# Kernel optimization log

Hardware: AMD Instinct MI355X
Metric: run time of the kernel (lower is better)

Reference implementation:

```python
import jax, jax.numpy as jnp
import numpy as np
from jax import lax

WINDOW = 512
HOP = 128
SR = 16000
ALPHA = 1e-06
F = WINDOW // 2 + 1  # 257 bins
GAIN = float(np.sqrt(8.0 / 3.0))

# frequency-domain constants (match PsychoacousticMasker properties)
_freqs = np.linspace(0.0, SR / 2.0, F)
_bark_np = 13.0 * np.arctan(0.00076 * _freqs) + 3.5 * np.arctan((_freqs / 7500.0) ** 2)
_valid_dom = (_freqs >= 20.0) & (_freqs <= 20000.0)
_ath_np = np.full(F, -np.inf)
_fk = _freqs[_valid_dom] * 0.001
_ath_np[_valid_dom] = 3.64 * _fk ** -0.8 - 6.5 * np.exp(-0.6 * (_fk - 3.3) ** 2) + 0.001 * _fk ** 4 - 12.0
BARK = jnp.asarray(_bark_np, jnp.float32)
ATH = jnp.asarray(_ath_np, jnp.float32)
DELTA_SHIFT = -6.025 - 0.275 * BARK
HANN = jnp.asarray(0.5 * (1.0 - np.cos(2.0 * np.pi * np.arange(WINDOW) / WINDOW)), jnp.float32)


def _stft(x):
    # center=False hann STFT -> [n_frames, F] complex
    n_frames = (x.shape[0] - WINDOW) // HOP + 1
    idx = jnp.arange(n_frames)[:, None] * HOP + jnp.arange(WINDOW)[None, :]
    return jnp.fft.rfft(x[idx] * HANN, axis=-1)


def _frame_threshold(p):
    # p: [F] SPL-normalized PSD (dB) for one frame -> global masking threshold [F]
    interior = (p[1:-1] > p[:-2]) & (p[1:-1] > p[2:])
    is_max = jnp.pad(interior, (1, 1), constant_values=False)
    pw = 10.0 ** (p / 10.0)
    m_all = 10.0 * jnp.log10(pw + jnp.roll(pw, 1) + jnp.roll(pw, -1))  # tonal masker level (bins j-1,j,j+1)
    valid = is_max & (m_all > ATH)
    order = jnp.argsort((~valid).astype(jnp.int32))  # stable: valid bins first, in frequency order
    vmask = valid[order]
    m_c = jnp.where(vmask, m_all[order], -200.0)     # compacted masker dB values
    n = valid.sum()

    def step(carry, i):
        i_prev, keep = carry
        active = i < n
        # NB: source indexes bark[] with masker *list positions* (i, i_prev); replicated faithfully
        close = (BARK[i] - BARK[i_prev]) < 0.5
        prev_smaller = m_c[i_prev] < m_c[i]
        del_idx = jnp.where(prev_smaller, i_prev, i)
        keep = jnp.where(active & close, keep.at[del_idx].set(False), keep)
        i_prev = jnp.where(active, jnp.where(close, jnp.where(prev_smaller, i_prev + 1, i_prev), i), i_prev)
        return (i_prev, keep), None

    (_, keep), _ = lax.scan(step, (jnp.int32(0), jnp.ones(F, dtype=bool)), jnp.arange(1, F, dtype=jnp.int32))
    keep = keep & vmask
    # individual thresholds, vectorized over maskers k and bins
    z_j = BARK[order]                                    # bark of each masker's bin
    dz = BARK[None, :] - z_j[:, None]                    # [K, F]
    slope = jnp.where(dz > 0, -27.0 + 0.37 * jnp.maximum(m_c - 40.0, 0.0)[:, None], 27.0)
    t = m_c[:, None] + DELTA_SHIFT[order][:, None] + slope * dz
    power = jnp.where(keep[:, None], 10.0 ** (t / 10.0), 0.0)
    return 10.0 * jnp.log10(power.sum(0) + 10.0 ** (ATH / 10.0))


def _threshold_and_psd_max(audio):
    s = _stft(audio)                                     # [T, F]
    psd = 20.0 * jnp.log10(jnp.abs(GAIN * s / WINDOW))
    psd = jnp.maximum(psd, -200.0)
    psd_max = psd.max()
    psd_n = 96.0 - psd_max + psd
    thr = jax.vmap(_frame_threshold)(psd_n)              # [T, F]
    return thr, psd_max


def setup_inputs() -> dict:
    key = jax.random.key(0)
    k1, k2 = jax.random.split(key)
    L = 160000  # 10 s @ 16 kHz; (L - 512) % 128 == 0 -> 1247 frames, pad is a no-op
    x_ref = 0.5 * jax.random.normal(k1, (L,), dtype=jnp.float32)
    x_adv = x_ref + 0.01 * jax.random.normal(k2, (L,), dtype=jnp.float32)
    return {"x_adv": x_adv, "x_ref": x_ref}


def reference(x_adv, x_ref):
    thr, psd_max = _threshold_and_psd_max(x_ref)
    thr = lax.stop_gradient(thr)
    psd_max = lax.stop_gradient(psd_max)
    delta = x_adv - x_ref
    sd = _stft(delta)                                    # [T, F]
    psd_d = (GAIN / WINDOW) ** 2 * (sd.real ** 2 + sd.imag ** 2)
    psd_d = (10.0 ** 9.6) / (10.0 ** (psd_max / 10.0)) * psd_d
    loss = jnp.mean(jax.nn.relu(psd_d - 10.0 ** (thr / 10.0)))
    return ALPHA * loss
```

## Files before the change

### kernel.cpp

```cpp
#include <hip/hip_runtime.h>
#include <math.h>


#define FBINS 257

#define TAB_BARK  0
#define TAB_ATHDB 257
#define TAB_ATHP  514
#define TAB_HANN  771
#define TAB_TWR   1283
#define TAB_TWI   1539
#define TAB_FLOATS 2048

__global__ __launch_bounds__(256) void k0_init(float* __restrict__ tab)
{
    const int tid = threadIdx.x;
    const double TWO_PI = 6.283185307179586476925286766559;
    for (int f = tid; f < FBINS; f += 256) {
        double freq = 31.25 * (double)f;
        double q    = freq / 7500.0;
        tab[TAB_BARK + f] = (float)(13.0 * atan(0.00076 * freq) + 3.5 * atan(q * q));
        if (f == 0) {
            tab[TAB_ATHDB] = -INFINITY;
            tab[TAB_ATHP]  = 0.0f;
        } else {
            double fk = freq * 0.001;
            double ad = 3.64 * pow(fk, -0.8)
                      - 6.5 * exp(-0.6 * (fk - 3.3) * (fk - 3.3))
                      + 0.001 * fk * fk * fk * fk - 12.0;
            float av = (float)ad;
            tab[TAB_ATHDB + f] = av;
            tab[TAB_ATHP  + f] = exp10f(av / 10.0f);
        }
    }
    for (int n = tid; n < 512; n += 256) {
        double cw = cos((TWO_PI * (double)n) / 512.0);
        tab[TAB_HANN + n] = (float)(0.5 * (1.0 - cw));
    }
    for (int j = tid; j < 256; j += 256) {
        double s, c;
        sincos(-(TWO_PI / 512.0) * (double)j, &s, &c);
        tab[TAB_TWR + j] = (float)c;
        tab[TAB_TWI + j] = (float)s;
    }
}

__global__ __launch_bounds__(256) void k1_stft(
    const float* __restrict__ xadv, const float* __restrict__ xref,
    const float* __restrict__ tab,
    float* __restrict__ psd_db, float* __restrict__ pd, float* __restrict__ fmaxs)
{
    __shared__ float re[512], im[512], twr[256], twi[256];
    __shared__ float wmax[4];
    const int t = blockIdx.x, tid = threadIdx.x;

    twr[tid] = tab[TAB_TWR + tid];
    twi[tid] = tab[TAB_TWI + tid];

    const int base_idx = t * 128;
    for (int n = tid; n < 512; n += 256) {
        float w = tab[TAB_HANN + n];
        float r = xref[base_idx + n];
        float a = xadv[base_idx + n];
        int   p = __brev((unsigned)n) >> 23;
        re[p] = w * r;
        im[p] = w * (a - r);
    }
    __syncthreads();

    for (int stage = 1; stage <= 9; ++stage) {
        int half  = 1 << (stage - 1);
        int tstep = 512 >> stage;
        int j     = tid & (half - 1);
        int base  = ((tid >> (stage - 1)) << stage) + j;
        float wr = twr[j * tstep], wi = twi[j * tstep];
        float vr0 = re[base + half], vi0 = im[base + half];
        float vr = vr0 * wr - vi0 * wi;
        float vi = vr0 * wi + vi0 * wr;
        float ur = re[base], ui = im[base];
        __syncthreads();
        re[base]        = ur + vr; im[base]        = ui + vi;
        re[base + half] = ur - vr; im[base + half] = ui - vi;
        __syncthreads();
    }

    const float S2 = 1.0172526041666667e-05f;
    float lmax = -1e30f;
    for (int k = tid; k <= 256; k += 256) {
        int nk = (512 - k) & 511;
        float zr = re[k],  zi = im[k];
        float yr = re[nk], yi = im[nk];
        float ar = 0.5f * (zr + yr), ai = 0.5f * (zi - yi);
        float br = 0.5f * (zi + yi), bi = 0.5f * (yr - zr);
        float prefp = S2 * (ar * ar + ai * ai);
        float pdb   = fmaxf(10.0f * log10f(prefp), -200.0f);
        psd_db[t * FBINS + k] = pdb;
        pd[t * FBINS + k]     = S2 * (br * br + bi * bi);
        lmax = fmaxf(lmax, pdb);
    }
    for (int off = 32; off > 0; off >>= 1) lmax = fmaxf(lmax, __shfl_down(lmax, off));
    if ((tid & 63) == 0) wmax[tid >> 6] = lmax;
    __syncthreads();
    if (tid == 0)
        fmaxs[t] = fmaxf(fmaxf(wmax[0], wmax[1]), fmaxf(wmax[2], wmax[3]));
}

__global__ __launch_bounds__(256) void k2_max(
    const float* __restrict__ fmaxs, int nf, float* __restrict__ psdmax)
{
    __shared__ float sm[4];
    float v = -1e30f;
    for (int i = threadIdx.x; i < nf; i += 256) v = fmaxf(v, fmaxs[i]);
    for (int off = 32; off > 0; off >>= 1) v = fmaxf(v, __shfl_down(v, off));
    if ((threadIdx.x & 63) == 0) sm[threadIdx.x >> 6] = v;
    __syncthreads();
    if (threadIdx.x == 0)
        psdmax[0] = fmaxf(fmaxf(sm[0], sm[1]), fmaxf(sm[2], sm[3]));
}

__global__ __launch_bounds__(256) void k3_threshold(
    const float* __restrict__ tab,
    const float* __restrict__ psd_db, const float* __restrict__ pd,
    const float* __restrict__ psdmax, float* __restrict__ floss)
{
    __shared__ float barkf[FBINS], athp_s[FBINS];
    __shared__ float p_s[FBINS], pw_s[FBINS];
    __shared__ float mc_s[128], shift_s[128], barkm_s[128], ups_s[128];
    __shared__ int   bin_s[128], keep_s[128];
    __shared__ int   wcnt[4];
    __shared__ float red[4];

    const int t = blockIdx.x, tid = threadIdx.x;
    const int lane = tid & 63, wid = tid >> 6;
    const float pmax   = psdmax[0];
    const float shift0 = 96.0f - pmax;

    for (int f = tid; f < FBINS; f += 256) {
        barkf[f]  = tab[TAB_BARK + f];
        athp_s[f] = tab[TAB_ATHP + f];
        float pv = shift0 + psd_db[t * FBINS + f];
        p_s[f]  = pv;
        pw_s[f] = exp10f(pv / 10.0f);
    }
    __syncthreads();

    float m = -1e30f;
    int   pred = 0;
    if (tid >= 1 && tid <= 255) {
        float pc = p_s[tid];
        if (pc > p_s[tid - 1] && pc > p_s[tid + 1]) {
            m = 10.0f * log10f((pw_s[tid] + pw_s[tid - 1]) + pw_s[tid + 1]);
            if (m > tab[TAB_ATHDB + tid]) pred = 1;
        }
    }
    unsigned long long bal = __ballot(pred);
    if (lane == 0) wcnt[wid] = __popcll(bal);
    __syncthreads();
    int base = 0;
    for (int w = 0; w < wid; ++w) base += wcnt[w];
    const int n_total = wcnt[0] + wcnt[1] + wcnt[2] + wcnt[3];
    if (pred) {
        int pos = base + __popcll(bal & ((1ull << lane) - 1));
        bin_s[pos] = tid; mc_s[pos] = m; keep_s[pos] = 1;
    }
    __syncthreads();

    if (tid == 0) {
        int i_prev = 0;
        for (int i = 1; i < n_total; ++i) {
            bool close        = (barkf[i] - barkf[i_prev]) < 0.5f;
            bool prev_smaller = mc_s[i_prev] < mc_s[i];
            if (close) {
                keep_s[prev_smaller ? i_prev : i] = 0;
                if (prev_smaller) i_prev = i_prev + 1;
            } else {
                i_prev = i;
            }
        }
    }
    __syncthreads();

    int pred2 = (tid < n_total) && keep_s[tid];
    unsigned long long bal2 = __ballot(pred2);
    if (lane == 0) wcnt[wid] = __popcll(bal2);
    __syncthreads();
    int base2 = 0;
    for (int w = 0; w < wid; ++w) base2 += wcnt[w];
    const int nk = wcnt[0] + wcnt[1] + wcnt[2] + wcnt[3];
    if (pred2) {
        int pos = base2 + __popcll(bal2 & ((1ull << lane) - 1));
        int   fb = bin_s[tid];
        float mc = mc_s[tid];
        shift_s[pos] = mc + (-6.025f - 0.275f * barkf[fb]);
        barkm_s[pos] = barkf[fb];
        ups_s[pos]   = -27.0f + 0.37f * fmaxf(mc - 40.0f, 0.0f);
    }
    __syncthreads();

    const float C = 3981071705.534973f / exp10f(pmax / 10.0f);
    float lsum = 0.0f;
    for (int f = tid; f < FBINS; f += 256) {
        float bf  = barkf[f];
        float acc = 0.0f;
        for (int k = 0; k < nk; ++k) {
            float dz    = bf - barkm_s[k];
            float slope = (dz > 0.0f) ? ups_s[k] : 27.0f;
            float tdb   = shift_s[k] + slope * dz;
            acc += exp10f(tdb / 10.0f);
        }
        float thrpow = acc + athp_s[f];
        float pds    = C * pd[t * FBINS + f];
        lsum += fmaxf(pds - thrpow, 0.0f);
    }
    for (int off = 32; off > 0; off >>= 1) lsum += __shfl_down(lsum, off);
    if ((tid & 63) == 0) red[tid >> 6] = lsum;
    __syncthreads();
    if (tid == 0) floss[t] = (red[0] + red[1]) + (red[2] + red[3]);
}

__global__ __launch_bounds__(256) void k4_final(
    const float* __restrict__ floss, int nf, float* __restrict__ out)
{
    __shared__ float red[4];
    float s = 0.0f;
    for (int i = threadIdx.x; i < nf; i += 256) s += floss[i];
    for (int off = 32; off > 0; off >>= 1) s += __shfl_down(s, off);
    if ((threadIdx.x & 63) == 0) red[threadIdx.x >> 6] = s;
    __syncthreads();
    if (threadIdx.x == 0) {
        float total = (red[0] + red[1]) + (red[2] + red[3]);
        out[0] = 1e-6f * (total / (float)(nf * FBINS));
    }
}

extern "C" void kernel_launch(void* const* d_in, const int* in_sizes, int n_in,
                              void* d_out, int out_size, void* d_ws, size_t ws_size,
                              hipStream_t stream)
{
    const float* x_adv = (const float*)d_in[0];
    const float* x_ref = (const float*)d_in[1];
    float*       out   = (float*)d_out;

    const int L  = in_sizes[0];
    const int nf = (L - 512) / 128 + 1;

    float* ws      = (float*)d_ws;
    float* tab     = ws;
    float* psd_db  = ws + TAB_FLOATS;
    float* pd      = psd_db + (size_t)nf * FBINS;
    float* fmaxs   = pd + (size_t)nf * FBINS;
    float* floss   = fmaxs + nf;
    float* psdmax  = floss + nf;

    k0_init     <<<1,  256, 0, stream>>>(tab);
    k1_stft     <<<nf, 256, 0, stream>>>(x_adv, x_ref, tab, psd_db, pd, fmaxs);
    k2_max      <<<1,  256, 0, stream>>>(fmaxs, nf, psdmax);
    k3_threshold<<<nf, 256, 0, stream>>>(tab, psd_db, pd, psdmax, floss);
    k4_final    <<<1,  256, 0, stream>>>(floss, nf, out);
}
```

Before: 93.29 us.

## Split init across blocks, ping-pong FFT buffers, pipeline serial masker scan

The table-init kernel now spreads its three independent table computations (bark/ATH, Hann window, twiddles) over three blocks instead of one. The STFT butterfly stages use double-buffered shared arrays, which removes one __syncthreads per stage. The single-thread masker pruning loop reads packed (bark, level) pairs and prefetches the next entry, shortening the serial dependency chain of shared-memory loads. Shared memory per block grows slightly in k1 and k3.

```diff
diff --git a/kernel.cpp b/kernel.cpp
--- a/kernel.cpp
+++ b/kernel.cpp
@@ -16,32 +16,36 @@
 {
     const int tid = threadIdx.x;
     const double TWO_PI = 6.283185307179586476925286766559;
-    for (int f = tid; f < FBINS; f += 256) {
-        double freq = 31.25 * (double)f;
-        double q    = freq / 7500.0;
-        tab[TAB_BARK + f] = (float)(13.0 * atan(0.00076 * freq) + 3.5 * atan(q * q));
-        if (f == 0) {
-            tab[TAB_ATHDB] = -INFINITY;
-            tab[TAB_ATHP]  = 0.0f;
-        } else {
-            double fk = freq * 0.001;
-            double ad = 3.64 * pow(fk, -0.8)
-                      - 6.5 * exp(-0.6 * (fk - 3.3) * (fk - 3.3))
-                      + 0.001 * fk * fk * fk * fk - 12.0;
-            float av = (float)ad;
-            tab[TAB_ATHDB + f] = av;
-            tab[TAB_ATHP  + f] = exp10f(av / 10.0f);
-        }
-    }
-    for (int n = tid; n < 512; n += 256) {
-        double cw = cos((TWO_PI * (double)n) / 512.0);
-        tab[TAB_HANN + n] = (float)(0.5 * (1.0 - cw));
-    }
-    for (int j = tid; j < 256; j += 256) {
-        double s, c;
-        sincos(-(TWO_PI / 512.0) * (double)j, &s, &c);
-        tab[TAB_TWR + j] = (float)c;
-        tab[TAB_TWI + j] = (float)s;
+    if (blockIdx.x == 0) {
+        for (int f = tid; f < FBINS; f += 256) {
+            double freq = 31.25 * (double)f;
+            double q    = freq / 7500.0;
+            tab[TAB_BARK + f] = (float)(13.0 * atan(0.00076 * freq) + 3.5 * atan(q * q));
+            if (f == 0) {
+                tab[TAB_ATHDB] = -INFINITY;
+                tab[TAB_ATHP]  = 0.0f;
+            } else {
+                double fk = freq * 0.001;
+                double ad = 3.64 * pow(fk, -0.8)
+                          - 6.5 * exp(-0.6 * (fk - 3.3) * (fk - 3.3))
+                          + 0.001 * fk * fk * fk * fk - 12.0;
+                float av = (float)ad;
+                tab[TAB_ATHDB + f] = av;
+                tab[TAB_ATHP  + f] = exp10f(av / 10.0f);
+            }
+        }
+    } else if (blockIdx.x == 1) {
+        for (int n = tid; n < 512; n += 256) {
+            double cw = cos((TWO_PI * (double)n) / 512.0);
+            tab[TAB_HANN + n] = (float)(0.5 * (1.0 - cw));
+        }
+    } else {
+        for (int j = tid; j < 256; j += 256) {
+            double s, c;
+            sincos(-(TWO_PI / 512.0) * (double)j, &s, &c);
+            tab[TAB_TWR + j] = (float)c;
+            tab[TAB_TWI + j] = (float)s;
+        }
     }
 }
 
@@ -50,7 +54,7 @@
     const float* __restrict__ tab,
     float* __restrict__ psd_db, float* __restrict__ pd, float* __restrict__ fmaxs)
 {
-    __shared__ float re[512], im[512], twr[256], twi[256];
+    __shared__ float re[2][512], im[2][512], twr[256], twi[256];
     __shared__ float wmax[4];
     const int t = blockIdx.x, tid = threadIdx.x;
 
@@ -63,24 +67,25 @@
         float r = xref[base_idx + n];
         float a = xadv[base_idx + n];
         int   p = __brev((unsigned)n) >> 23;
-        re[p] = w * r;
-        im[p] = w * (a - r);
-    }
-    __syncthreads();
-
+        re[0][p] = w * r;
+        im[0][p] = w * (a - r);
+    }
+    __syncthreads();
+
+    int cur = 0;
     for (int stage = 1; stage <= 9; ++stage) {
         int half  = 1 << (stage - 1);
         int tstep = 512 >> stage;
         int j     = tid & (half - 1);
         int base  = ((tid >> (stage - 1)) << stage) + j;
         float wr = twr[j * tstep], wi = twi[j * tstep];
-        float vr0 = re[base + half], vi0 = im[base + half];
+        float vr0 = re[cur][base + half], vi0 = im[cur][base + half];
         float vr = vr0 * wr - vi0 * wi;
         float vi = vr0 * wi + vi0 * wr;
-        float ur = re[base], ui = im[base];
-        __syncthreads();
-        re[base]        = ur + vr; im[base]        = ui + vi;
-        re[base + half] = ur - vr; im[base + half] = ui - vi;
+        float ur = re[cur][base], ui = im[cur][base];
+        re[cur ^ 1][base]        = ur + vr; im[cur ^ 1][base]        = ui + vi;
+        re[cur ^ 1][base + half] = ur - vr; im[cur ^ 1][base + half] = ui - vi;
+        cur ^= 1;
         __syncthreads();
     }
 
@@ -88,8 +93,8 @@
     float lmax = -1e30f;
     for (int k = tid; k <= 256; k += 256) {
         int nk = (512 - k) & 511;
-        float zr = re[k],  zi = im[k];
-        float yr = re[nk], yi = im[nk];
+        float zr = re[cur][k],  zi = im[cur][k];
+        float yr = re[cur][nk], yi = im[cur][nk];
         float ar = 0.5f * (zr + yr), ai = 0.5f * (zi - yi);
         float br = 0.5f * (zi + yi), bi = 0.5f * (yr - zr);
         float prefp = S2 * (ar * ar + ai * ai);
@@ -127,6 +132,7 @@
     __shared__ float p_s[FBINS], pw_s[FBINS];
     __shared__ float mc_s[128], shift_s[128], barkm_s[128], ups_s[128];
     __shared__ int   bin_s[128], keep_s[128];
+    __shared__ float2 pmk[132];
     __shared__ int   wcnt[4];
     __shared__ float red[4];
 
@@ -165,17 +171,31 @@
     }
     __syncthreads();
 
-    if (tid == 0) {
-        int i_prev = 0;
+    if (tid <= n_total && tid < 130) {
+        pmk[tid] = (tid < n_total) ? make_float2(barkf[tid], mc_s[tid])
+                                   : make_float2(1.0e30f, -1.0e30f);
+    }
+    __syncthreads();
+
+    if (tid == 0 && n_total > 1) {
+        int   i_prev = 0;
+        float bp = pmk[0].x, mp = pmk[0].y;
+        float2 c = pmk[1];
         for (int i = 1; i < n_total; ++i) {
-            bool close        = (barkf[i] - barkf[i_prev]) < 0.5f;
-            bool prev_smaller = mc_s[i_prev] < mc_s[i];
+            float2 nx = pmk[i + 1];
+            bool close        = (c.x - bp) < 0.5f;
+            bool prev_smaller = mp < c.y;
             if (close) {
                 keep_s[prev_smaller ? i_prev : i] = 0;
-                if (prev_smaller) i_prev = i_prev + 1;
+                if (prev_smaller) {
+                    ++i_prev;
+                    if (i_prev == i) { bp = c.x; mp = c.y; }
+                    else { float2 p = pmk[i_prev]; bp = p.x; mp = p.y; }
+                }
             } else {
-                i_prev = i;
+                i_prev = i; bp = c.x; mp = c.y;
             }
+            c = nx;
         }
     }
     __syncthreads();
@@ -252,7 +272,7 @@
     float* floss   = fmaxs + nf;
     float* psdmax  = floss + nf;
 
-    k0_init     <<<1,  256, 0, stream>>>(tab);
+    k0_init     <<<3,  256, 0, stream>>>(tab);
     k1_stft     <<<nf, 256, 0, stream>>>(x_adv, x_ref, tab, psd_db, pd, fmaxs);
     k2_max      <<<1,  256, 0, stream>>>(fmaxs, nf, psdmax);
     k3_threshold<<<nf, 256, 0, stream>>>(tab, psd_db, pd, psdmax, floss);
```

New measurement: 89.25 us. 4.3% less time.
